# Kernel optimization log

Hardware: AMD Instinct MI355X
Metric: run time of the kernel (lower is better)

Reference implementation:

```python
import jax, jax.numpy as jnp
import numpy as np

D_MODEL = 512
NUM_HEADS = 8


def setup_inputs() -> dict:
    key = jax.random.key(0)
    ks = jax.random.split(key, 12)
    B, S, D = 2, 4096, D_MODEL
    s = 1.0 / np.sqrt(D)
    return {
        "q": jax.random.normal(ks[0], (B, S, D), jnp.float32),
        "k": jax.random.normal(ks[1], (B, S, D), jnp.float32),
        "v": jax.random.normal(ks[2], (B, S, D), jnp.float32),
        "w_q": jax.random.normal(ks[3], (D, D), jnp.float32) * s,
        "b_q": jax.random.normal(ks[4], (D,), jnp.float32) * s,
        "w_k": jax.random.normal(ks[5], (D, D), jnp.float32) * s,
        "b_k": jax.random.normal(ks[6], (D,), jnp.float32) * s,
        "w_v": jax.random.normal(ks[7], (D, D), jnp.float32) * s,
        "b_v": jax.random.normal(ks[8], (D,), jnp.float32) * s,
        "w_o": jax.random.normal(ks[9], (D, D), jnp.float32) * s,
        "b_o": jax.random.normal(ks[10], (D,), jnp.float32) * s,
    }


def _split(x, num_heads):
    B, S, D = x.shape
    return x.reshape(B, S, num_heads, D // num_heads).transpose(0, 2, 1, 3)


def reference(q, k, v, w_q, b_q, w_k, b_k, w_v, b_v, w_o, b_o):
    # Linear projections (torch Linear: x @ W^T + b)
    qp = q @ w_q.T + b_q
    kp = k @ w_k.T + b_k
    vp = v @ w_v.T + b_v
    # split into heads: [B, H, S, d_head]
    qh = _split(qp, NUM_HEADS)
    kh = _split(kp, NUM_HEADS)
    vh = _split(vp, NUM_HEADS)
    d_head = qh.shape[-1]
    # NOTE: original scales by sqrt(d_model of the per-head tensor) == sqrt(d_head)
    score = jnp.einsum("bhqd,bhkd->bhqk", qh, kh) / jnp.sqrt(jnp.float32(d_head))
    attn = jax.nn.softmax(score, axis=-1)  # full [B,H,S,S] materialized, as in source
    out = jnp.einsum("bhqk,bhkd->bhqd", attn, vh)
    # concat heads back to [B, S, D]
    B, H, S, Dh = out.shape
    out = out.transpose(0, 2, 1, 3).reshape(B, S, H * Dh)
    return out @ w_o.T + b_o
```

## Files before the change

### kernel.cpp

```cpp
#include <hip/hip_runtime.h>
#include <math.h>

typedef __bf16 bf16_t;
typedef __bf16 bf16x4_v __attribute__((ext_vector_type(4)));
typedef __bf16 bf16x8_t __attribute__((ext_vector_type(8)));
typedef float f32x4_t __attribute__((ext_vector_type(4)));
typedef unsigned uint2_t __attribute__((ext_vector_type(2)));
typedef unsigned uint4_t __attribute__((ext_vector_type(4)));

#define S_LEN 4096
#define DM 512
#define NH 8
#define DH 64
#define MTOT 8192

#define Q_SCALE 0.1803368801111204f

#define REG   4194304
#define WREG  262144
#define W_OFF (3 * REG)
#define CVT_TOTAL (3 * REG + 4 * WREG)
#define QH_OFF CVT_TOTAL

__device__ inline f32x4_t mfma16(bf16x8_t a, bf16x8_t b, f32x4_t c) {
    return __builtin_amdgcn_mfma_f32_16x16x32_bf16(a, b, c, 0, 0, 0);
}

__device__ inline unsigned pkbf16(float a, float b) {
    unsigned short ra = __builtin_bit_cast(unsigned short, (bf16_t)a);
    unsigned short rb = __builtin_bit_cast(unsigned short, (bf16_t)b);
    return (unsigned)ra | ((unsigned)rb << 16);
}

__device__ inline void async_copy16(const void* g, void* l) {
    __builtin_amdgcn_global_load_lds(
        (const __attribute__((address_space(1))) void*)g,
        (__attribute__((address_space(3))) void*)l, 16, 0, 0);
}

__global__ __launch_bounds__(256) void cvt_all(
    const float* __restrict__ q, const float* __restrict__ k, const float* __restrict__ v,
    const float* __restrict__ wq, const float* __restrict__ wk,
    const float* __restrict__ wv, const float* __restrict__ wo,
    bf16_t* __restrict__ dst)
{
    long gidx = (long)blockIdx.x * 2048 + (long)threadIdx.x * 8;
    const float* src;
    long off = gidx;
    if      (gidx < 1L * REG)          { src = q; }
    else if (gidx < 2L * REG)          { src = k;  off = gidx - 1L * REG; }
    else if (gidx < 3L * REG)          { src = v;  off = gidx - 2L * REG; }
    else if (gidx < W_OFF + 1L * WREG) { src = wq; off = gidx - W_OFF; }
    else if (gidx < W_OFF + 2L * WREG) { src = wk; off = gidx - (W_OFF + 1L * WREG); }
    else if (gidx < W_OFF + 3L * WREG) { src = wv; off = gidx - (W_OFF + 2L * WREG); }
    else                               { src = wo; off = gidx - (W_OFF + 3L * WREG); }
    float4 a = *(const float4*)(src + off);
    float4 b = *(const float4*)(src + off + 4);
    bf16x8_t h;
    h[0] = (bf16_t)a.x; h[1] = (bf16_t)a.y; h[2] = (bf16_t)a.z; h[3] = (bf16_t)a.w;
    h[4] = (bf16_t)b.x; h[5] = (bf16_t)b.y; h[6] = (bf16_t)b.z; h[7] = (bf16_t)b.w;
    *(bf16x8_t*)(dst + gidx) = h;
}

__global__ __launch_bounds__(256) void gemm_qkv(
    const bf16_t* __restrict__ XWb,
    const float* __restrict__ B0, const float* __restrict__ B1, const float* __restrict__ B2,
    bf16_t* __restrict__ dst_base)
{
    const int p = blockIdx.z;
    const bf16_t* __restrict__ X = XWb + (size_t)p * REG;
    const bf16_t* __restrict__ W = XWb + W_OFF + (size_t)p * WREG;
    const float* __restrict__ Bi = (p == 0) ? B0 : ((p == 1) ? B1 : B2);
    bf16_t* __restrict__ dst = dst_base + (size_t)p * REG;

    const int m0 = blockIdx.x * 128;
    const int n0 = blockIdx.y * 128;
    const int tid = threadIdx.x;
    const int lane = tid & 63, wid = tid >> 6;
    const int lm = lane & 15, lg = lane >> 4;
    const int wm = (wid >> 1) * 64, wn = (wid & 1) * 64;

    __shared__ __align__(16) bf16_t smemAB[2][128 * 64];
    bf16_t* As = smemAB[0];
    bf16_t* Bs = smemAB[1];

    f32x4_t acc[4][4] = {};

    const int r0 = tid >> 3, c7 = tid & 7;
    const int cA0 = ((lg) ^ (lm & 7)) * 8;
    const int cA1 = ((4 + lg) ^ (lm & 7)) * 8;

    for (int kb = 0; kb < DM / 64; ++kb) {
        const int k0 = kb * 64;
#pragma unroll
        for (int i = 0; i < 4; ++i) {
            int row = i * 32 + r0;
            int ch = c7 ^ (row & 7);
            async_copy16(X + (size_t)(m0 + row) * DM + k0 + ch * 8, (char*)As + (i * 256 + tid) * 16);
            async_copy16(W + (size_t)(n0 + row) * DM + k0 + ch * 8, (char*)Bs + (i * 256 + tid) * 16);
        }
        __syncthreads();
#pragma unroll
        for (int kd = 0; kd < 2; ++kd) {
            const int co = kd ? cA1 : cA0;
            bf16x8_t fa[4], fb[4];
#pragma unroll
            for (int mt = 0; mt < 4; ++mt) {
                fa[mt] = *(const bf16x8_t*)(As + (wm + mt * 16 + lm) * 64 + co);
                fb[mt] = *(const bf16x8_t*)(Bs + (wn + mt * 16 + lm) * 64 + co);
            }
            if (p < 2) {
#pragma unroll
                for (int mt = 0; mt < 4; ++mt)
#pragma unroll
                    for (int nt = 0; nt < 4; ++nt)
                        acc[nt][mt] = mfma16(fb[nt], fa[mt], acc[nt][mt]);
            } else {
#pragma unroll
                for (int mt = 0; mt < 4; ++mt)
#pragma unroll
                    for (int nt = 0; nt < 4; ++nt)
                        acc[mt][nt] = mfma16(fa[mt], fb[nt], acc[mt][nt]);
            }
        }
        __syncthreads();
    }

    if (p == 2) {
        bf16_t* tb = &smemAB[0][0];
#pragma unroll
        for (int nt = 0; nt < 4; ++nt) {
            int colL = wn + nt * 16 + lm;
            float bv = Bi[n0 + colL];
#pragma unroll
            for (int mt = 0; mt < 4; ++mt) {
                int sL = wm + mt * 16 + lg * 4;
                bf16x4_v pk;
#pragma unroll
                for (int r = 0; r < 4; ++r) pk[r] = (bf16_t)(acc[mt][nt][r] + bv);
                int byte = colL * 256 + ((((sL >> 3) ^ (colL & 15))) * 16) + (sL & 7) * 2;
                *(bf16x4_v*)((char*)tb + byte) = pk;
            }
        }
        __syncthreads();
        {
            const int colL = tid >> 1, half = tid & 1;
            const int col = n0 + colL;
            const int h = (col >> 6) & 7, dc = col & 63;
            const int bb = m0 >> 12, s0 = m0 & (S_LEN - 1);
            size_t base = (((size_t)(bb * NH + h)) * DH + dc) * S_LEN + s0;
#pragma unroll
            for (int j = 0; j < 8; ++j) {
                int chunk = half * 8 + j;
                bf16x8_t v = *(const bf16x8_t*)((char*)tb + colL * 256 + ((chunk ^ (colL & 15)) * 16));
                *(bf16x8_t*)&dst[base + chunk * 8] = v;
            }
        }
    } else {
        const float scale = (p == 0) ? Q_SCALE : 1.0f;
#pragma unroll
        for (int nt = 0; nt < 4; ++nt) {
            int ncol = n0 + wn + nt * 16 + lg * 4;
            float4 bv4 = *(const float4*)&Bi[ncol];
            int h = (ncol >> 6) & 7, dc = ncol & 63;
#pragma unroll
            for (int mt = 0; mt < 4; ++mt) {
                int m = m0 + wm + mt * 16 + lm;
                int bb = m >> 12, s = m & (S_LEN - 1);
                bf16x4_v pk;
                pk[0] = (bf16_t)((acc[nt][mt][0] + bv4.x) * scale);
                pk[1] = (bf16_t)((acc[nt][mt][1] + bv4.y) * scale);
                pk[2] = (bf16_t)((acc[nt][mt][2] + bv4.z) * scale);
                pk[3] = (bf16_t)((acc[nt][mt][3] + bv4.w) * scale);
                *(bf16x4_v*)&dst[(((size_t)(bb * NH + h)) * S_LEN + s) * DH + dc] = pk;
            }
        }
    }
}

__global__ __launch_bounds__(256, 2) void flash_attn(
    const bf16_t* __restrict__ Qh, const bf16_t* __restrict__ Kh,
    const bf16_t* __restrict__ Vth, bf16_t* __restrict__ O)
{
    const int bh = blockIdx.y;
    const int q0 = blockIdx.x * 128;
    const int tid = threadIdx.x;
    const int lane = tid & 63, wid = tid >> 6;
    const int lm = lane & 15, lg = lane >> 4;
    const int qg = wid & 1;
    const int kvh = wid >> 1;

    const bf16_t* __restrict__ Qb  = Qh  + (size_t)bh * S_LEN * DH;
    const bf16_t* __restrict__ Kb  = Kh  + (size_t)bh * S_LEN * DH;
    const bf16_t* __restrict__ Vtg = Vth + (size_t)bh * S_LEN * DH;

    __shared__ __align__(16) char smem[65536];

    bf16x8_t bQ[4][2];
#pragma unroll
    for (int nt = 0; nt < 4; ++nt)
#pragma unroll
        for (int kd = 0; kd < 2; ++kd)
            bQ[nt][kd] = *(const bf16x8_t*)(Qb + (size_t)(q0 + qg * 64 + nt * 16 + lm) * DH + kd * 32 + lg * 8);

    f32x4_t o_acc[4][4] = {};
    f32x4_t l4[4] = {};

    const uint4_t onesu = {0x3F803F80u, 0x3F803F80u, 0x3F803F80u, 0x3F803F80u};
    const bf16x8_t vOnes = __builtin_bit_cast(bf16x8_t, onesu);

    const int srow = tid >> 3;
    const int slch = (tid & 7) ^ (srow & 7);
    const bf16_t* gK = Kb + (size_t)srow * DH + slch * 8;
    const bf16_t* gV = Vtg + (size_t)srow * S_LEN + slch * 8;

    const int cK0 = ((lg) ^ (lm & 7)) * 16;
    const int cK1 = ((4 + lg) ^ (lm & 7)) * 16;

    {
        char* b = smem;
#pragma unroll
        for (int i = 0; i < 4; ++i)
            async_copy16(gK + (size_t)(32 * i) * DH, b + i * 4096 + tid * 16);
#pragma unroll
        for (int i = 0; i < 4; ++i)
            async_copy16(gV + (size_t)(i & 1) * 32 * S_LEN + (i >> 1) * 64,
                         b + 16384 + i * 4096 + tid * 16);
    }

    const int NT = S_LEN / 128;
    for (int it = 0; it < NT; ++it) {
        const char* buf = smem + (it & 1) * 32768;
        __syncthreads();

        if (it + 1 < NT) {
            char* nb = smem + ((it + 1) & 1) * 32768;
            const int kvb = (it + 1) * 128;
#pragma unroll
            for (int i = 0; i < 4; ++i)
                async_copy16(gK + (size_t)(kvb + 32 * i) * DH, nb + i * 4096 + tid * 16);
#pragma unroll
            for (int i = 0; i < 4; ++i)
                async_copy16(gV + (size_t)(i & 1) * 32 * S_LEN + kvb + (i >> 1) * 64,
                             nb + 16384 + i * 4096 + tid * 16);
        }

        const char* ksb = buf + kvh * 8192;
        const char* vsb = buf + 16384 + kvh * 8192;

        uint4_t pq[2][4];
#pragma unroll
        for (int mt = 0; mt < 4; ++mt) {
            const char* krow = ksb + (mt * 16 + lm) * 128;
            bf16x8_t aK0 = *(const bf16x8_t*)(krow + cK0);
            bf16x8_t aK1 = *(const bf16x8_t*)(krow + cK1);
            const int cc = mt >> 1, hf = (mt & 1) * 2;
#pragma unroll
            for (int nt = 0; nt < 4; ++nt) {
                f32x4_t s = {};
                s = mfma16(aK0, bQ[nt][0], s);
                s = mfma16(aK1, bQ[nt][1], s);
                float e0 = __builtin_amdgcn_exp2f(s[0]);
                float e1 = __builtin_amdgcn_exp2f(s[1]);
                float e2 = __builtin_amdgcn_exp2f(s[2]);
                float e3 = __builtin_amdgcn_exp2f(s[3]);
                pq[cc][nt][hf + 0] = pkbf16(e0, e1);
                pq[cc][nt][hf + 1] = pkbf16(e2, e3);
            }
        }

#pragma unroll
        for (int cc = 0; cc < 2; ++cc)
#pragma unroll
            for (int nt = 0; nt < 4; ++nt)
                l4[nt] = mfma16(vOnes, __builtin_bit_cast(bf16x8_t, pq[cc][nt]), l4[nt]);

#pragma unroll
        for (int mt = 0; mt < 4; ++mt) {
            const char* vrow = vsb + (mt * 16 + lm) * 128;
#pragma unroll
            for (int cc = 0; cc < 2; ++cc) {
                const int ca = 2 * cc, cb = 2 * cc + 1;
                int pc0 = (ca * 2 + (lg >> 1)) ^ (lm & 7);
                int pc1 = (cb * 2 + (lg >> 1)) ^ (lm & 7);
                uint2_t va0 = *(const uint2_t*)(vrow + pc0 * 16 + (lg & 1) * 8);
                uint2_t va1 = *(const uint2_t*)(vrow + pc1 * 16 + (lg & 1) * 8);
                bf16x8_t vA = __builtin_bit_cast(bf16x8_t, (uint4_t){va0[0], va0[1], va1[0], va1[1]});
#pragma unroll
                for (int nt = 0; nt < 4; ++nt)
                    o_acc[mt][nt] = mfma16(vA, __builtin_bit_cast(bf16x8_t, pq[cc][nt]), o_acc[mt][nt]);
            }
        }
    }

    __syncthreads();

    float* ob = (float*)smem + qg * (64 * 68);
    float* lb = (float*)(smem + 34816);

    if (kvh == 1) {
#pragma unroll
        for (int nt = 0; nt < 4; ++nt) {
#pragma unroll
            for (int mt = 0; mt < 4; ++mt)
                *(f32x4_t*)&ob[(nt * 16 + lm) * 68 + mt * 16 + lg * 4] = o_acc[mt][nt];
            if (lg == 0) lb[qg * 64 + nt * 16 + lm] = l4[nt][0];
        }
    }
    __syncthreads();
    if (kvh == 0) {
        const int bb = bh >> 3, h = bh & 7;
#pragma unroll
        for (int nt = 0; nt < 4; ++nt) {
            float ltot = l4[nt][0] + lb[qg * 64 + nt * 16 + lm];
            float inv = 1.0f / ltot;
            int q = q0 + qg * 64 + nt * 16 + lm;
            size_t base = ((size_t)(bb * S_LEN + q)) * DM + h * DH;
#pragma unroll
            for (int mt = 0; mt < 4; ++mt) {
                f32x4_t orow = *(const f32x4_t*)&ob[(nt * 16 + lm) * 68 + mt * 16 + lg * 4];
                bf16x4_v pkd;
#pragma unroll
                for (int r = 0; r < 4; ++r)
                    pkd[r] = (bf16_t)((o_acc[mt][nt][r] + orow[r]) * inv);
                *(bf16x4_v*)&O[base + mt * 16 + lg * 4] = pkd;
            }
        }
    }
}

__global__ __launch_bounds__(256) void gemm_out(
    const bf16_t* __restrict__ A, const bf16_t* __restrict__ W,
    const float* __restrict__ Bi, float* __restrict__ out)
{
    const int m0 = blockIdx.x * 64;
    const int n0 = blockIdx.y * 128;
    const int tid = threadIdx.x;
    const int lane = tid & 63, wid = tid >> 6;
    const int lm = lane & 15, lg = lane >> 4;
    const int wm = (wid >> 1) * 32, wn = (wid & 1) * 64;

    __shared__ __align__(16) bf16_t As[64 * 64];
    __shared__ __align__(16) bf16_t Bs[128 * 64];

    f32x4_t acc[4][2] = {};

    const int r0 = tid >> 3, c7 = tid & 7;
    const int cA0 = ((lg) ^ (lm & 7)) * 8;
    const int cA1 = ((4 + lg) ^ (lm & 7)) * 8;

    for (int kb = 0; kb < DM / 64; ++kb) {
        const int k0 = kb * 64;
#pragma unroll
        for (int i = 0; i < 2; ++i) {
            int idx = i * 256 + tid;
            int row = idx >> 3;
            int ch = (idx & 7) ^ (row & 7);
            async_copy16(A + (size_t)(m0 + row) * DM + k0 + ch * 8, (char*)As + idx * 16);
        }
#pragma unroll
        for (int i = 0; i < 4; ++i) {
            int row = i * 32 + r0;
            int ch = c7 ^ (row & 7);
            async_copy16(W + (size_t)(n0 + row) * DM + k0 + ch * 8, (char*)Bs + (i * 256 + tid) * 16);
        }
        __syncthreads();
#pragma unroll
        for (int kd = 0; kd < 2; ++kd) {
            const int co = kd ? cA1 : cA0;
            bf16x8_t fa[2], fb[4];
#pragma unroll
            for (int mt = 0; mt < 2; ++mt)
                fa[mt] = *(const bf16x8_t*)(As + (wm + mt * 16 + lm) * 64 + co);
#pragma unroll
            for (int nt = 0; nt < 4; ++nt)
                fb[nt] = *(const bf16x8_t*)(Bs + (wn + nt * 16 + lm) * 64 + co);
#pragma unroll
            for (int nt = 0; nt < 4; ++nt)
#pragma unroll
                for (int mt = 0; mt < 2; ++mt)
                    acc[nt][mt] = mfma16(fb[nt], fa[mt], acc[nt][mt]);
        }
        __syncthreads();
    }

#pragma unroll
    for (int nt = 0; nt < 4; ++nt) {
        int ncol = n0 + wn + nt * 16 + lg * 4;
        float4 bv4 = *(const float4*)&Bi[ncol];
#pragma unroll
        for (int mt = 0; mt < 2; ++mt) {
            int m = m0 + wm + mt * 16 + lm;
            float4 ov;
            ov.x = acc[nt][mt][0] + bv4.x;
            ov.y = acc[nt][mt][1] + bv4.y;
            ov.z = acc[nt][mt][2] + bv4.z;
            ov.w = acc[nt][mt][3] + bv4.w;
            *(float4*)&out[(size_t)m * DM + ncol] = ov;
        }
    }
}

extern "C" void kernel_launch(void* const* d_in, const int* in_sizes, int n_in,
                              void* d_out, int out_size, void* d_ws, size_t ws_size,
                              hipStream_t stream)
{
    const float* q  = (const float*)d_in[0];
    const float* k  = (const float*)d_in[1];
    const float* v  = (const float*)d_in[2];
    const float* wq = (const float*)d_in[3];
    const float* bq = (const float*)d_in[4];
    const float* wk = (const float*)d_in[5];
    const float* bk = (const float*)d_in[6];
    const float* wv = (const float*)d_in[7];
    const float* bv = (const float*)d_in[8];
    const float* wo = (const float*)d_in[9];
    const float* bo = (const float*)d_in[10];
    float* out = (float*)d_out;

    bf16_t* ws = (bf16_t*)d_ws;
    bf16_t* XWb = ws;
    bf16_t* Qh  = ws + QH_OFF;
    bf16_t* Kh  = Qh + REG;
    bf16_t* VTh = Kh + REG;
    bf16_t* Ob  = ws;
    bf16_t* Wob = ws + W_OFF + 3 * (size_t)WREG;

    cvt_all<<<CVT_TOTAL / 2048, 256, 0, stream>>>(q, k, v, wq, wk, wv, wo, XWb);

    dim3 g1(MTOT / 128, DM / 128, 3);
    gemm_qkv<<<g1, 256, 0, stream>>>(XWb, bq, bk, bv, Qh);

    dim3 g2(S_LEN / 128, 2 * NH, 1);
    flash_attn<<<g2, 256, 0, stream>>>(Qh, Kh, VTh, Ob);

    dim3 g3(MTOT / 64, DM / 128, 1);
    gemm_out<<<g3, 256, 0, stream>>>(Ob, Wob, bo, out);
}
```

Baseline: 219.3 us.

## Halve KV tile to 64 rows and raise flash-attention occupancy to four blocks

Shrinks the per-iteration KV tile in the flash attention kernel from 128 to 64 keys, cutting double-buffered LDS from 64KB to 36KB. Launch bounds go from 2 to 4 blocks per CU. The P register footprint shrinks from pq[2][4] to pq[4], and the V fragment indexing is reworked so each KV-half wave reads its own 32-key slice. The aim is more waves resident to hide latency, at the cost of twice as many loop iterations and barriers and tighter register limits that may cause spills.

Measured after the change: 465.1 us. +112.1%, slower.

```diff
diff --git a/kernel.cpp b/kernel.cpp
--- a/kernel.cpp
+++ b/kernel.cpp
@@ -178,7 +178,7 @@
     }
 }
 
-__global__ __launch_bounds__(256, 2) void flash_attn(
+__global__ __launch_bounds__(256, 4) void flash_attn(
     const bf16_t* __restrict__ Qh, const bf16_t* __restrict__ Kh,
     const bf16_t* __restrict__ Vth, bf16_t* __restrict__ O)
 {
@@ -194,7 +194,7 @@
     const bf16_t* __restrict__ Kb  = Kh  + (size_t)bh * S_LEN * DH;
     const bf16_t* __restrict__ Vtg = Vth + (size_t)bh * S_LEN * DH;
 
-    __shared__ __align__(16) char smem[65536];
+    __shared__ __align__(16) char smem[36864];
 
     bf16x8_t bQ[4][2];
 #pragma unroll
@@ -216,45 +216,40 @@
 
     const int cK0 = ((lg) ^ (lm & 7)) * 16;
     const int cK1 = ((4 + lg) ^ (lm & 7)) * 16;
+    const int qoff = kvh * 4;
 
     {
         char* b = smem;
-#pragma unroll
-        for (int i = 0; i < 4; ++i)
-            async_copy16(gK + (size_t)(32 * i) * DH, b + i * 4096 + tid * 16);
-#pragma unroll
-        for (int i = 0; i < 4; ++i)
-            async_copy16(gV + (size_t)(i & 1) * 32 * S_LEN + (i >> 1) * 64,
-                         b + 16384 + i * 4096 + tid * 16);
-    }
-
-    const int NT = S_LEN / 128;
+        async_copy16(gK, b + tid * 16);
+        async_copy16(gK + (size_t)32 * DH, b + 4096 + tid * 16);
+        async_copy16(gV, b + 8192 + tid * 16);
+        async_copy16(gV + (size_t)32 * S_LEN, b + 12288 + tid * 16);
+    }
+
+    const int NT = S_LEN / 64;
     for (int it = 0; it < NT; ++it) {
-        const char* buf = smem + (it & 1) * 32768;
+        const char* buf = smem + (it & 1) * 16384;
         __syncthreads();
 
         if (it + 1 < NT) {
-            char* nb = smem + ((it + 1) & 1) * 32768;
-            const int kvb = (it + 1) * 128;
-#pragma unroll
-            for (int i = 0; i < 4; ++i)
-                async_copy16(gK + (size_t)(kvb + 32 * i) * DH, nb + i * 4096 + tid * 16);
-#pragma unroll
-            for (int i = 0; i < 4; ++i)
-                async_copy16(gV + (size_t)(i & 1) * 32 * S_LEN + kvb + (i >> 1) * 64,
-                             nb + 16384 + i * 4096 + tid * 16);
-        }
-
-        const char* ksb = buf + kvh * 8192;
-        const char* vsb = buf + 16384 + kvh * 8192;
-
-        uint4_t pq[2][4];
-#pragma unroll
-        for (int mt = 0; mt < 4; ++mt) {
+            char* nb = smem + ((it + 1) & 1) * 16384;
+            const int kvb = (it + 1) * 64;
+            async_copy16(gK + (size_t)kvb * DH, nb + tid * 16);
+            async_copy16(gK + (size_t)(kvb + 32) * DH, nb + 4096 + tid * 16);
+            async_copy16(gV + kvb, nb + 8192 + tid * 16);
+            async_copy16(gV + (size_t)32 * S_LEN + kvb, nb + 12288 + tid * 16);
+        }
+
+        const char* ksb = buf + kvh * 4096;
+        const char* vsb = buf + 8192;
+
+        uint4_t pq[4];
+#pragma unroll
+        for (int mt = 0; mt < 2; ++mt) {
             const char* krow = ksb + (mt * 16 + lm) * 128;
             bf16x8_t aK0 = *(const bf16x8_t*)(krow + cK0);
             bf16x8_t aK1 = *(const bf16x8_t*)(krow + cK1);
-            const int cc = mt >> 1, hf = (mt & 1) * 2;
+            const int hf = mt * 2;
 #pragma unroll
             for (int nt = 0; nt < 4; ++nt) {
                 f32x4_t s = {};
@@ -264,32 +259,26 @@
                 float e1 = __builtin_amdgcn_exp2f(s[1]);
                 float e2 = __builtin_amdgcn_exp2f(s[2]);
                 float e3 = __builtin_amdgcn_exp2f(s[3]);
-                pq[cc][nt][hf + 0] = pkbf16(e0, e1);
-                pq[cc][nt][hf + 1] = pkbf16(e2, e3);
-            }
-        }
-
-#pragma unroll
-        for (int cc = 0; cc < 2; ++cc)
-#pragma unroll
-            for (int nt = 0; nt < 4; ++nt)
-                l4[nt] = mfma16(vOnes, __builtin_bit_cast(bf16x8_t, pq[cc][nt]), l4[nt]);
+                pq[nt][hf + 0] = pkbf16(e0, e1);
+                pq[nt][hf + 1] = pkbf16(e2, e3);
+            }
+        }
+
+#pragma unroll
+        for (int nt = 0; nt < 4; ++nt)
+            l4[nt] = mfma16(vOnes, __builtin_bit_cast(bf16x8_t, pq[nt]), l4[nt]);
 
 #pragma unroll
         for (int mt = 0; mt < 4; ++mt) {
             const char* vrow = vsb + (mt * 16 + lm) * 128;
-#pragma unroll
-            for (int cc = 0; cc < 2; ++cc) {
-                const int ca = 2 * cc, cb = 2 * cc + 1;
-                int pc0 = (ca * 2 + (lg >> 1)) ^ (lm & 7);
-                int pc1 = (cb * 2 + (lg >> 1)) ^ (lm & 7);
-                uint2_t va0 = *(const uint2_t*)(vrow + pc0 * 16 + (lg & 1) * 8);
-                uint2_t va1 = *(const uint2_t*)(vrow + pc1 * 16 + (lg & 1) * 8);
-                bf16x8_t vA = __builtin_bit_cast(bf16x8_t, (uint4_t){va0[0], va0[1], va1[0], va1[1]});
-#pragma unroll
-                for (int nt = 0; nt < 4; ++nt)
-                    o_acc[mt][nt] = mfma16(vA, __builtin_bit_cast(bf16x8_t, pq[cc][nt]), o_acc[mt][nt]);
-            }
+            int pc0 = (qoff + 0 + (lg >> 1)) ^ (lm & 7);
+            int pc1 = (qoff + 2 + (lg >> 1)) ^ (lm & 7);
+            uint2_t va0 = *(const uint2_t*)(vrow + pc0 * 16 + (lg & 1) * 8);
+            uint2_t va1 = *(const uint2_t*)(vrow + pc1 * 16 + (lg & 1) * 8);
+            bf16x8_t vA = __builtin_bit_cast(bf16x8_t, (uint4_t){va0[0], va0[1], va1[0], va1[1]});
+#pragma unroll
+            for (int nt = 0; nt < 4; ++nt)
+                o_acc[mt][nt] = mfma16(vA, __builtin_bit_cast(bf16x8_t, pq[nt]), o_acc[mt][nt]);
         }
     }
 
```

## Double-buffer shared-memory tiles in QKV and output projection GEMMs

Applied to the files above, without the earlier changes.

Both projection GEMMs now use two shared-memory stages. The next K-tile is prefetched with async copies right after the barrier, while MFMA work runs on the current tile. This is meant to hide global-load latency behind compute and removes one barrier per K iteration. The cost is doubled LDS use (64 KB in gemm_qkv, 48 KB in gemm_out), which may reduce how many blocks fit per CU.

New measurement: 216.7 us. Within noise of the previous version (-1.2%).

```diff
diff --git a/kernel.cpp b/kernel.cpp
--- a/kernel.cpp
+++ b/kernel.cpp
@@ -80,9 +80,7 @@
     const int lm = lane & 15, lg = lane >> 4;
     const int wm = (wid >> 1) * 64, wn = (wid & 1) * 64;
 
-    __shared__ __align__(16) bf16_t smemAB[2][128 * 64];
-    bf16_t* As = smemAB[0];
-    bf16_t* Bs = smemAB[1];
+    __shared__ __align__(16) char gsmem[65536];
 
     f32x4_t acc[4][4] = {};
 
@@ -90,16 +88,29 @@
     const int cA0 = ((lg) ^ (lm & 7)) * 8;
     const int cA1 = ((4 + lg) ^ (lm & 7)) * 8;
 
+#pragma unroll
+    for (int i = 0; i < 4; ++i) {
+        int row = i * 32 + r0;
+        int ch = c7 ^ (row & 7);
+        async_copy16(X + (size_t)(m0 + row) * DM + ch * 8, gsmem + (i * 256 + tid) * 16);
+        async_copy16(W + (size_t)(n0 + row) * DM + ch * 8, gsmem + 16384 + (i * 256 + tid) * 16);
+    }
+
     for (int kb = 0; kb < DM / 64; ++kb) {
-        const int k0 = kb * 64;
-#pragma unroll
-        for (int i = 0; i < 4; ++i) {
-            int row = i * 32 + r0;
-            int ch = c7 ^ (row & 7);
-            async_copy16(X + (size_t)(m0 + row) * DM + k0 + ch * 8, (char*)As + (i * 256 + tid) * 16);
-            async_copy16(W + (size_t)(n0 + row) * DM + k0 + ch * 8, (char*)Bs + (i * 256 + tid) * 16);
-        }
         __syncthreads();
+        if (kb + 1 < DM / 64) {
+            const int k0 = (kb + 1) * 64;
+            char* nb = gsmem + ((kb + 1) & 1) * 32768;
+#pragma unroll
+            for (int i = 0; i < 4; ++i) {
+                int row = i * 32 + r0;
+                int ch = c7 ^ (row & 7);
+                async_copy16(X + (size_t)(m0 + row) * DM + k0 + ch * 8, nb + (i * 256 + tid) * 16);
+                async_copy16(W + (size_t)(n0 + row) * DM + k0 + ch * 8, nb + 16384 + (i * 256 + tid) * 16);
+            }
+        }
+        const bf16_t* As = (const bf16_t*)(gsmem + (kb & 1) * 32768);
+        const bf16_t* Bs = (const bf16_t*)(gsmem + (kb & 1) * 32768 + 16384);
 #pragma unroll
         for (int kd = 0; kd < 2; ++kd) {
             const int co = kd ? cA1 : cA0;
@@ -123,11 +134,11 @@
                         acc[mt][nt] = mfma16(fa[mt], fb[nt], acc[mt][nt]);
             }
         }
+    }
+
+    if (p == 2) {
         __syncthreads();
-    }
-
-    if (p == 2) {
-        bf16_t* tb = &smemAB[0][0];
+        bf16_t* tb = (bf16_t*)gsmem;
 #pragma unroll
         for (int nt = 0; nt < 4; ++nt) {
             int colL = wn + nt * 16 + lm;
@@ -340,8 +351,7 @@
     const int lm = lane & 15, lg = lane >> 4;
     const int wm = (wid >> 1) * 32, wn = (wid & 1) * 64;
 
-    __shared__ __align__(16) bf16_t As[64 * 64];
-    __shared__ __align__(16) bf16_t Bs[128 * 64];
+    __shared__ __align__(16) char gsmem[49152];
 
     f32x4_t acc[4][2] = {};
 
@@ -349,22 +359,41 @@
     const int cA0 = ((lg) ^ (lm & 7)) * 8;
     const int cA1 = ((4 + lg) ^ (lm & 7)) * 8;
 
+#pragma unroll
+    for (int i = 0; i < 2; ++i) {
+        int idx = i * 256 + tid;
+        int row = idx >> 3;
+        int ch = (idx & 7) ^ (row & 7);
+        async_copy16(A + (size_t)(m0 + row) * DM + ch * 8, gsmem + idx * 16);
+    }
+#pragma unroll
+    for (int i = 0; i < 4; ++i) {
+        int row = i * 32 + r0;
+        int ch = c7 ^ (row & 7);
+        async_copy16(W + (size_t)(n0 + row) * DM + ch * 8, gsmem + 8192 + (i * 256 + tid) * 16);
+    }
+
     for (int kb = 0; kb < DM / 64; ++kb) {
-        const int k0 = kb * 64;
-#pragma unroll
-        for (int i = 0; i < 2; ++i) {
-            int idx = i * 256 + tid;
-            int row = idx >> 3;
-            int ch = (idx & 7) ^ (row & 7);
-            async_copy16(A + (size_t)(m0 + row) * DM + k0 + ch * 8, (char*)As + idx * 16);
-        }
-#pragma unroll
-        for (int i = 0; i < 4; ++i) {
-            int row = i * 32 + r0;
-            int ch = c7 ^ (row & 7);
-            async_copy16(W + (size_t)(n0 + row) * DM + k0 + ch * 8, (char*)Bs + (i * 256 + tid) * 16);
-        }
         __syncthreads();
+        if (kb + 1 < DM / 64) {
+            const int k0 = (kb + 1) * 64;
+            char* nb = gsmem + ((kb + 1) & 1) * 24576;
+#pragma unroll
+            for (int i = 0; i < 2; ++i) {
+                int idx = i * 256 + tid;
+                int row = idx >> 3;
+                int ch = (idx & 7) ^ (row & 7);
+                async_copy16(A + (size_t)(m0 + row) * DM + k0 + ch * 8, nb + idx * 16);
+            }
+#pragma unroll
+            for (int i = 0; i < 4; ++i) {
+                int row = i * 32 + r0;
+                int ch = c7 ^ (row & 7);
+                async_copy16(W + (size_t)(n0 + row) * DM + k0 + ch * 8, nb + 8192 + (i * 256 + tid) * 16);
+            }
+        }
+        const bf16_t* As = (const bf16_t*)(gsmem + (kb & 1) * 24576);
+        const bf16_t* Bs = (const bf16_t*)(gsmem + (kb & 1) * 24576 + 8192);
 #pragma unroll
         for (int kd = 0; kd < 2; ++kd) {
             const int co = kd ? cA1 : cA0;
@@ -381,7 +410,6 @@
                 for (int mt = 0; mt < 2; ++mt)
                     acc[nt][mt] = mfma16(fb[nt], fa[mt], acc[nt][mt]);
         }
-        __syncthreads();
     }
 
 #pragma unroll
```
